# Kernel optimization log

Measured on AMD Instinct MI355X. Metric: run time of the kernel, lower is better.

The kernel has to match this reference:

```python
import jax, jax.numpy as jnp
import numpy as np
import math

B, S, D, H, MLP, L = 4, 1024, 512, 8, 2048, 4
C = D // H  # head dim = 64
K_RATIO = 0.25
TOPK = max(1, min(S, int(math.ceil(K_RATIO * S))))  # 256
EPS = 1e-6


def layernorm(x, w, b):
    mu = jnp.mean(x, axis=-1, keepdims=True)
    var = jnp.mean(jnp.square(x - mu), axis=-1, keepdims=True)
    return (x - mu) * jax.lax.rsqrt(var + EPS) * w + b


def dwconv3(x, w):
    # x: (B, Ch, S), w: (Ch, 1, 3) depthwise conv, padding 1
    return jax.lax.conv_general_dilated(
        x, w, window_strides=(1,), padding=[(1, 1)],
        dimension_numbers=('NCH', 'OIH', 'NCH'),
        feature_group_count=x.shape[1])


def setup_inputs() -> dict:
    key = jax.random.key(0)
    ks = jax.random.split(key, 16)
    g = lambda k, shape, s=0.02: jax.random.normal(k, shape, jnp.float32) * s
    return {
        'x': jax.random.normal(ks[0], (B, S, D), jnp.float32),
        'pos_emb': g(ks[1], (1, S, D)),
        'ln1_w': jnp.ones((L, D), jnp.float32),
        'ln1_b': jnp.zeros((L, D), jnp.float32),
        'qkv_w': g(ks[2], (L, 3 * D, D)),
        'dw_w': g(ks[3], (L, 3 * D, 1, 3), 0.1),
        'temp': jnp.ones((L, H), jnp.float32),
        'proj_w': g(ks[4], (L, D, D)),
        'ln2_w': jnp.ones((L, D), jnp.float32),
        'ln2_b': jnp.zeros((L, D), jnp.float32),
        'mlp_w1': g(ks[5], (L, MLP, D)),
        'mlp_b1': g(ks[6], (L, MLP), 1e-6),
        'mlp_w2': g(ks[7], (L, D, MLP)),
        'mlp_b2': g(ks[8], (L, D), 1e-6),
        'lnf_w': jnp.ones((D,), jnp.float32),
        'lnf_b': jnp.zeros((D,), jnp.float32),
    }


def _block(x, ln1_w, ln1_b, qkv_w, dw_w, temp, proj_w, ln2_w, ln2_b,
           mlp_w1, mlp_b1, mlp_w2, mlp_b2):
    # x: (B, S, D)
    h = layernorm(x, ln1_w, ln1_b).swapaxes(1, 2)        # (B, D, S)
    qkv = jnp.einsum('od,bds->bos', qkv_w, h)            # (B, 3D, S) 1x1 conv
    qkv = dwconv3(qkv, dw_w)                             # depthwise k=3
    q, k, v = jnp.split(qkv, 3, axis=1)                  # each (B, D, S)
    # 'b (head c) s -> b head s c'
    to_heads = lambda t: t.reshape(B, H, C, S).transpose(0, 1, 3, 2)
    q, k, v = to_heads(q), to_heads(k), to_heads(v)      # (B, H, S, C)
    q = q / jnp.maximum(jnp.linalg.norm(q, axis=-1, keepdims=True), 1e-12)
    k = k / jnp.maximum(jnp.linalg.norm(k, axis=-1, keepdims=True), 1e-12)
    scores = jnp.einsum('bhsc,bhtc->bhst', q, k) * temp[None, :, None, None]
    # top-k per query row: keep entries >= k-th largest, mask rest to -inf
    kth = jax.lax.top_k(scores, TOPK)[0][..., -1:]       # (B, H, S, 1)
    sparse = jnp.where(scores >= kth, scores, -jnp.inf)
    sparse = jnp.clip(sparse, -10000.0, 10000.0)         # -inf -> -10000
    attn = jax.nn.softmax(sparse, axis=-1)
    out = jnp.einsum('bhst,bhtc->bhsc', attn, v)         # (B, H, S, C)
    out = out.transpose(0, 1, 3, 2).reshape(B, D, S)     # 'b head s c -> b (head c) s'
    out = jnp.einsum('od,bds->bos', proj_w, out)         # project_out 1x1 conv
    x = x + out.swapaxes(1, 2)                           # residual (dropout=0)
    y = layernorm(x, ln2_w, ln2_b)
    y = jax.nn.gelu(y @ mlp_w1.T + mlp_b1, approximate=False) @ mlp_w2.T + mlp_b2
    return x + y


def reference(x, pos_emb, ln1_w, ln1_b, qkv_w, dw_w, temp, proj_w,
              ln2_w, ln2_b, mlp_w1, mlp_b1, mlp_w2, mlp_b2, lnf_w, lnf_b):
    h = x + pos_emb
    for i in range(L):
        h = _block(h, ln1_w[i], ln1_b[i], qkv_w[i], dw_w[i], temp[i], proj_w[i],
                   ln2_w[i], ln2_b[i], mlp_w1[i], mlp_b1[i], mlp_w2[i], mlp_b2[i])
    return layernorm(h, lnf_w, lnf_b)
```

## Files before the change

kernel.cpp:

```cpp
#include <hip/hip_runtime.h>

#define NB   4
#define SEQ  1024
#define DIM  512
#define NH   8
#define HD   64
#define MLPD 2048
#define NL   4
#define TOPKK 256
#define QKVD 1536
#define QT   16

typedef short bh8 __attribute__((ext_vector_type(8)));
typedef float f32x4 __attribute__((ext_vector_type(4)));

__device__ __forceinline__ float b2f(unsigned short v) {
    return __uint_as_float(((unsigned)v) << 16);
}
__device__ __forceinline__ unsigned short f2b(float f) {
    unsigned u = __float_as_uint(f);
    u += 0x7FFFu + ((u >> 16) & 1u);
    return (unsigned short)(u >> 16);
}
__device__ __forceinline__ float ldin(const void* p, size_t i, int bf) {
    return bf ? b2f(((const unsigned short*)p)[i]) : ((const float*)p)[i];
}
__device__ __forceinline__ float wave_sum(float v) {
#pragma unroll
    for (int m = 32; m; m >>= 1) v += __shfl_xor(v, m);
    return v;
}
__device__ __forceinline__ unsigned f2key16(unsigned short u) {
    return (u & 0x8000u) ? (unsigned)((~u) & 0xFFFFu) : (unsigned)(u | 0x8000u);
}
__device__ __forceinline__ unsigned short key16b(unsigned k) {
    return (k & 0x8000u) ? (unsigned short)(k & 0x7FFFu)
                         : (unsigned short)((~k) & 0xFFFFu);
}
__device__ __forceinline__ uint4 pack8(const float* __restrict__ p) {
    uint4 r;
    r.x = (unsigned)f2b(p[0]) | ((unsigned)f2b(p[1]) << 16);
    r.y = (unsigned)f2b(p[2]) | ((unsigned)f2b(p[3]) << 16);
    r.z = (unsigned)f2b(p[4]) | ((unsigned)f2b(p[5]) << 16);
    r.w = (unsigned)f2b(p[6]) | ((unsigned)f2b(p[7]) << 16);
    return r;
}
__device__ __forceinline__ void async16(unsigned short* lds, const unsigned short* g) {
    __builtin_amdgcn_global_load_lds(
        (const __attribute__((address_space(1))) unsigned int*)g,
        (__attribute__((address_space(3))) unsigned int*)lds, 16, 0, 0);
}


__global__ void detect_kernel(const unsigned short* __restrict__ ln1w,
                              int* __restrict__ flag) {
    if (threadIdx.x == 0 && blockIdx.x == 0)
        *flag = (ln1w[0] == 0x3F80u) ? 1 : 0;
}

__global__ __launch_bounds__(256) void wcvt_kernel(
    const void* __restrict__ W, unsigned short* __restrict__ out,
    int n, const int* __restrict__ dflag) {
    int bf = *dflag;
    int idx = blockIdx.x * 256 + threadIdx.x;
    if (idx < n) out[idx] = f2b(ldin(W, idx, bf));
}

__global__ __launch_bounds__(256) void addpos_kernel(
    const void* __restrict__ x, const void* __restrict__ pos,
    float* __restrict__ h, const int* __restrict__ dflag) {
    int bf = *dflag;
    int idx = blockIdx.x * 256 + threadIdx.x;
    int sd = idx & (SEQ * DIM - 1);
    h[idx] = ldin(x, idx, bf) + ldin(pos, sd, bf);
}

__global__ __launch_bounds__(256) void ln_kernel(
    const float* __restrict__ in, const void* __restrict__ w,
    const void* __restrict__ bb, size_t wo, unsigned short* __restrict__ out,
    const int* __restrict__ dflag) {
    int bf = *dflag;
    __shared__ float red[4];
    int row = blockIdx.x, tid = threadIdx.x;
    int lane = tid & 63, wid = tid >> 6;
    const float* p = in + (size_t)row * DIM;
    float x0 = p[tid], x1 = p[tid + 256];
    float s = wave_sum(x0 + x1);
    if (!lane) red[wid] = s;
    __syncthreads();
    float mean = (red[0] + red[1] + red[2] + red[3]) * (1.0f / DIM);
    float d0 = x0 - mean, d1 = x1 - mean;
    float q = wave_sum(d0 * d0 + d1 * d1);
    __syncthreads();
    if (!lane) red[wid] = q;
    __syncthreads();
    float var = (red[0] + red[1] + red[2] + red[3]) * (1.0f / DIM);
    float rs = rsqrtf(var + 1e-6f);
    unsigned short* o = out + (size_t)row * DIM;
    o[tid]       = f2b(d0 * rs * ldin(w, wo + tid, bf) + ldin(bb, wo + tid, bf));
    o[tid + 256] = f2b(d1 * rs * ldin(w, wo + tid + 256, bf) + ldin(bb, wo + tid + 256, bf));
}

__global__ __launch_bounds__(256) void lnf_kernel(
    const float* __restrict__ in, const void* __restrict__ w,
    const void* __restrict__ bb, void* __restrict__ out,
    const int* __restrict__ dflag) {
    int bf = *dflag;
    __shared__ float red[4];
    int row = blockIdx.x, tid = threadIdx.x;
    int lane = tid & 63, wid = tid >> 6;
    const float* p = in + (size_t)row * DIM;
    float x0 = p[tid], x1 = p[tid + 256];
    float s = wave_sum(x0 + x1);
    if (!lane) red[wid] = s;
    __syncthreads();
    float mean = (red[0] + red[1] + red[2] + red[3]) * (1.0f / DIM);
    float d0 = x0 - mean, d1 = x1 - mean;
    float q = wave_sum(d0 * d0 + d1 * d1);
    __syncthreads();
    if (!lane) red[wid] = q;
    __syncthreads();
    float var = (red[0] + red[1] + red[2] + red[3]) * (1.0f / DIM);
    float rs = rsqrtf(var + 1e-6f);
    float v0 = d0 * rs * ldin(w, tid, bf) + ldin(bb, tid, bf);
    float v1 = d1 * rs * ldin(w, tid + 256, bf) + ldin(bb, tid + 256, bf);
    size_t o = (size_t)row * DIM;
    if (bf) {
        ((unsigned short*)out)[o + tid]       = f2b(v0);
        ((unsigned short*)out)[o + tid + 256] = f2b(v1);
    } else {
        ((float*)out)[o + tid]       = v0;
        ((float*)out)[o + tid + 256] = v1;
    }
}

__global__ __launch_bounds__(256) void gemm_mfma_kernel(
    const unsigned short* __restrict__ A, const void* __restrict__ W, size_t wo,
    const void* __restrict__ bias, size_t bo, void* __restrict__ C,
    int M, int N, int K, int flags, const int* __restrict__ dflag) {
    int bf = *dflag;
    __shared__ unsigned short As[128 * 32];
    __shared__ unsigned short Bs[128 * 32];
    int tid = threadIdx.x;
    int w = tid >> 6, l = tid & 63;
    int n0 = blockIdx.x * 128, m0 = blockIdx.y * 128;
    int wm = (w >> 1) * 64, wn = (w & 1) * 64;
    int lq = l & 15, lk = l >> 4;

    int srow = w * 32 + (l >> 2);
    int cb = (l & 3) * 8;
    const unsigned short* aG = A + (size_t)(m0 + srow) * K + cb;
    size_t wb = wo + (size_t)(n0 + srow) * K + cb;
    unsigned short* sA0 = &As[w * 1024 + l * 8];
    unsigned short* sA1 = &As[w * 1024 + 512 + l * 8];
    unsigned short* sB0 = &Bs[w * 1024 + l * 8];
    unsigned short* sB1 = &Bs[w * 1024 + 512 + l * 8];

    f32x4 acc[4][4];
#pragma unroll
    for (int i = 0; i < 4; ++i)
#pragma unroll
        for (int j = 0; j < 4; ++j)
            acc[i][j] = (f32x4){0.f, 0.f, 0.f, 0.f};

    for (int k0 = 0; k0 < K; k0 += 32) {
        uint4 a0 = *(const uint4*)(aG + k0);
        uint4 a1 = *(const uint4*)(aG + 16 * K + k0);
        uint4 b0, b1;
        if (bf) {
            b0 = *(const uint4*)((const unsigned short*)W + wb + k0);
            b1 = *(const uint4*)((const unsigned short*)W + wb + 16 * K + k0);
        } else {
            b0 = pack8((const float*)W + wb + k0);
            b1 = pack8((const float*)W + wb + 16 * K + k0);
        }
        __syncthreads();
        *(uint4*)sA0 = a0;
        *(uint4*)sA1 = a1;
        *(uint4*)sB0 = b0;
        *(uint4*)sB1 = b1;
        __syncthreads();
        bh8 af[4], bw[4];
#pragma unroll
        for (int i = 0; i < 4; ++i) {
            af[i] = *(const bh8*)&As[(wm + i * 16 + lq) * 32 + lk * 8];
            bw[i] = *(const bh8*)&Bs[(wn + i * 16 + lq) * 32 + lk * 8];
        }
#pragma unroll
        for (int i = 0; i < 4; ++i)
#pragma unroll
            for (int j = 0; j < 4; ++j)
                acc[i][j] = __builtin_amdgcn_mfma_f32_16x16x32_bf16(
                    af[i], bw[j], acc[i][j], 0, 0, 0);
    }

    int lr4 = lk * 4;
#pragma unroll
    for (int i = 0; i < 4; ++i) {
#pragma unroll
        for (int j = 0; j < 4; ++j) {
            int n = n0 + wn + j * 16 + lq;
            float bv = (flags & 4) ? ldin(bias, bo + n, bf) : 0.0f;
#pragma unroll
            for (int r = 0; r < 4; ++r) {
                int m = m0 + wm + i * 16 + lr4 + r;
                float v = acc[i][j][r] + bv;
                if (flags & 2) v = 0.5f * v * (1.0f + erff(v * 0.70710678118654752f));
                size_t o = (size_t)m * N + n;
                if (flags & 1) ((float*)C)[o] += v;
                else           ((unsigned short*)C)[o] = f2b(v);
            }
        }
    }
}

__global__ __launch_bounds__(256) void gemm_mfma_n64_kernel(
    const unsigned short* __restrict__ A, const void* __restrict__ W, size_t wo,
    const void* __restrict__ bias, size_t bo, void* __restrict__ C,
    int M, int N, int K, int flags, const int* __restrict__ dflag) {
    int bf = *dflag;
    __shared__ unsigned short As[128 * 32];
    __shared__ unsigned short Bs[64 * 32];
    int tid = threadIdx.x;
    int w = tid >> 6, l = tid & 63;
    int n0 = blockIdx.x * 64, m0 = blockIdx.y * 128;
    int wm = (w >> 1) * 64, wn = (w & 1) * 32;
    int lq = l & 15, lk = l >> 4;

    int srowA = w * 32 + (l >> 2);
    int cb = (l & 3) * 8;
    const unsigned short* aG = A + (size_t)(m0 + srowA) * K + cb;
    int srowB = w * 16 + (l >> 2);
    size_t wb = wo + (size_t)(n0 + srowB) * K + cb;
    unsigned short* sA0 = &As[w * 1024 + l * 8];
    unsigned short* sA1 = &As[w * 1024 + 512 + l * 8];
    unsigned short* sB0 = &Bs[w * 512 + l * 8];

    f32x4 acc[4][2];
#pragma unroll
    for (int i = 0; i < 4; ++i) {
        acc[i][0] = (f32x4){0.f, 0.f, 0.f, 0.f};
        acc[i][1] = (f32x4){0.f, 0.f, 0.f, 0.f};
    }

    for (int k0 = 0; k0 < K; k0 += 32) {
        uint4 a0 = *(const uint4*)(aG + k0);
        uint4 a1 = *(const uint4*)(aG + 16 * K + k0);
        uint4 b0;
        if (bf) b0 = *(const uint4*)((const unsigned short*)W + wb + k0);
        else    b0 = pack8((const float*)W + wb + k0);
        __syncthreads();
        *(uint4*)sA0 = a0;
        *(uint4*)sA1 = a1;
        *(uint4*)sB0 = b0;
        __syncthreads();
        bh8 af[4], bw[2];
#pragma unroll
        for (int i = 0; i < 4; ++i)
            af[i] = *(const bh8*)&As[(wm + i * 16 + lq) * 32 + lk * 8];
        bw[0] = *(const bh8*)&Bs[(wn + lq) * 32 + lk * 8];
        bw[1] = *(const bh8*)&Bs[(wn + 16 + lq) * 32 + lk * 8];
#pragma unroll
        for (int i = 0; i < 4; ++i) {
            acc[i][0] = __builtin_amdgcn_mfma_f32_16x16x32_bf16(af[i], bw[0], acc[i][0], 0, 0, 0);
            acc[i][1] = __builtin_amdgcn_mfma_f32_16x16x32_bf16(af[i], bw[1], acc[i][1], 0, 0, 0);
        }
    }

    int lr4 = lk * 4;
#pragma unroll
    for (int i = 0; i < 4; ++i) {
#pragma unroll
        for (int j = 0; j < 2; ++j) {
            int n = n0 + wn + j * 16 + lq;
            float bv = (flags & 4) ? ldin(bias, bo + n, bf) : 0.0f;
#pragma unroll
            for (int r = 0; r < 4; ++r) {
                int m = m0 + wm + i * 16 + lr4 + r;
                float v = acc[i][j][r] + bv;
                if (flags & 2) v = 0.5f * v * (1.0f + erff(v * 0.70710678118654752f));
                size_t o = (size_t)m * N + n;
                if (flags & 1) ((float*)C)[o] += v;
                else           ((unsigned short*)C)[o] = f2b(v);
            }
        }
    }
}

__global__ __launch_bounds__(256) void gemm_n64_dlds_kernel(
    const unsigned short* __restrict__ A, const unsigned short* __restrict__ W, size_t wo,
    const void* __restrict__ bias, size_t bo, void* __restrict__ C,
    int M, int N, int K, int flags, const int* __restrict__ dflag) {
    __shared__ unsigned short As[128 * 32];
    __shared__ unsigned short Bs[64 * 32];
    int tid = threadIdx.x;
    int w = tid >> 6, l = tid & 63;
    int n0 = blockIdx.x * 64, m0 = blockIdx.y * 128;
    int kz = blockIdx.z;
    int Ks = K / (int)gridDim.z;
    int kbeg = kz * Ks, kend = kbeg + Ks;
    int wm = (w >> 1) * 64, wn = (w & 1) * 32;
    int lq = l & 15, lk = l >> 4;

    int srowA = w * 32 + (l >> 2);
    int srowB = w * 16 + (l >> 2);
    int cb = (l & 3) * 8;
    const unsigned short* aG = A + (size_t)(m0 + srowA) * K + cb;
    const unsigned short* wG = W + wo + (size_t)(n0 + srowB) * K + cb;
    unsigned short* lA0 = As + w * 1024;
    unsigned short* lA1 = As + w * 1024 + 512;
    unsigned short* lB0 = Bs + w * 512;

    f32x4 acc[4][2];
#pragma unroll
    for (int i = 0; i < 4; ++i) {
        acc[i][0] = (f32x4){0.f, 0.f, 0.f, 0.f};
        acc[i][1] = (f32x4){0.f, 0.f, 0.f, 0.f};
    }

    for (int k0 = kbeg; k0 < kend; k0 += 32) {
        __syncthreads();
        async16(lA0, aG + k0);
        async16(lA1, aG + 16 * K + k0);
        async16(lB0, wG + k0);
        __syncthreads();
        bh8 af[4], bw[2];
#pragma unroll
        for (int i = 0; i < 4; ++i)
            af[i] = *(const bh8*)&As[(wm + i * 16 + lq) * 32 + lk * 8];
        bw[0] = *(const bh8*)&Bs[(wn + lq) * 32 + lk * 8];
        bw[1] = *(const bh8*)&Bs[(wn + 16 + lq) * 32 + lk * 8];
#pragma unroll
        for (int i = 0; i < 4; ++i) {
            acc[i][0] = __builtin_amdgcn_mfma_f32_16x16x32_bf16(af[i], bw[0], acc[i][0], 0, 0, 0);
            acc[i][1] = __builtin_amdgcn_mfma_f32_16x16x32_bf16(af[i], bw[1], acc[i][1], 0, 0, 0);
        }
    }

    int bf = (flags & 4) ? *dflag : 0;
    int lr4 = lk * 4;
#pragma unroll
    for (int i = 0; i < 4; ++i) {
#pragma unroll
        for (int j = 0; j < 2; ++j) {
            int n = n0 + wn + j * 16 + lq;
            float bv = ((flags & 4) && kz == 0) ? ldin(bias, bo + n, bf) : 0.0f;
#pragma unroll
            for (int r = 0; r < 4; ++r) {
                int m = m0 + wm + i * 16 + lr4 + r;
                float v = acc[i][j][r] + bv;
                if (flags & 2) v = 0.5f * v * (1.0f + erff(v * 0.70710678118654752f));
                size_t o = (size_t)m * N + n;
                if (flags & 8)      atomicAdd(&((float*)C)[o], v);
                else if (flags & 1) ((float*)C)[o] += v;
                else                ((unsigned short*)C)[o] = f2b(v);
            }
        }
    }
}

__global__ __launch_bounds__(256) void dwqkv_kernel(
    const unsigned short* __restrict__ in, const void* __restrict__ w, size_t wo,
    const void* __restrict__ temp, size_t to,
    unsigned short* __restrict__ qn, unsigned short* __restrict__ Kc,
    unsigned short* __restrict__ Vt, const int* __restrict__ dflag) {
    int bf = *dflag;
    int tid = threadIdx.x;
    int g = tid >> 6, c = tid & 63;
    int gid = blockIdx.x * 4 + g;
    int h = gid & 7;
    int bs = gid >> 3;
    int s = bs & (SEQ - 1), b = bs >> 10;
    int bh = b * NH + h;
    const unsigned short* row = in + (size_t)bs * QKVD;
    float vals[3];
#pragma unroll
    for (int t = 0; t < 3; ++t) {
        int o = t * 512 + h * HD + c;
        float w0 = ldin(w, wo + o * 3 + 0, bf);
        float w1 = ldin(w, wo + o * 3 + 1, bf);
        float w2 = ldin(w, wo + o * 3 + 2, bf);
        float a = w1 * b2f(row[o]);
        if (s > 0)       a += w0 * b2f(row[o - QKVD]);
        if (s < SEQ - 1) a += w2 * b2f(row[o + QKVD]);
        vals[t] = a;
    }
    float qs = wave_sum(vals[0] * vals[0]);
    float ks = wave_sum(vals[1] * vals[1]);
    float t_ = ldin(temp, to + h, bf);
    qn[(size_t)bs * DIM + h * HD + c] = f2b(vals[0] / fmaxf(sqrtf(qs), 1e-12f) * t_);
    Kc[((size_t)bh * SEQ + s) * HD + c] = f2b(vals[1] / fmaxf(sqrtf(ks), 1e-12f));
    Vt[(((size_t)bh * 32 + (s >> 5)) * HD + c) * 32 + (s & 31)] = f2b(vals[2]);
}

__global__ __launch_bounds__(256) void attn_kernel(
    const unsigned short* __restrict__ q, const unsigned short* __restrict__ Kc,
    const unsigned short* __restrict__ Vt, unsigned short* __restrict__ outp) {
    __shared__ __align__(16) unsigned short sc16[QT * 1024];

    int tid = threadIdx.x;
    int w = tid >> 6, l = tid & 63;
    int lq = l & 15, lk = l >> 4;
    int bid = blockIdx.x;
    int qt = bid & 63;
    int h = (bid >> 6) & 7;
    int b = bid >> 9;
    int bh = b * NH + h;

    const unsigned short* qp = q + (size_t)(b * SEQ + qt * QT + lq) * DIM + h * HD + lk * 8;
    bh8 aq0 = *(const bh8*)(qp);
    bh8 aq1 = *(const bh8*)(qp + 32);

    const unsigned short* Kbh = Kc + (size_t)bh * SEQ * HD;
    int wi = lq & 7;
    for (int kb = 0; kb < 16; ++kb) {
        int key0 = (w * 16 + kb) * 16;
        const unsigned short* kp = Kbh + (size_t)(key0 + lq) * HD + lk * 8;
        bh8 b0 = *(const bh8*)(kp);
        bh8 b1 = *(const bh8*)(kp + 32);
        f32x4 acc = {0.f, 0.f, 0.f, 0.f};
        acc = __builtin_amdgcn_mfma_f32_16x16x32_bf16(aq0, b0, acc, 0, 0, 0);
        acc = __builtin_amdgcn_mfma_f32_16x16x32_bf16(aq1, b1, acc, 0, 0, 0);
        int chunk = (key0 + lq) >> 3;
#pragma unroll
        for (int r = 0; r < 4; ++r) {
            int row = lk * 4 + r;
            int sw = (row ^ (row >> 2)) & 7;
            sc16[row * 1024 + ((chunk ^ sw) << 3) + wi] = f2b(acc[r]);
        }
    }
    __syncthreads();

    for (int rr = 0; rr < 4; ++rr) {
        int row = w * 4 + rr;
        unsigned short* srow = sc16 + row * 1024;
        uint4 r0 = *(const uint4*)&srow[l * 8];
        uint4 r1 = *(const uint4*)&srow[512 + l * 8];
        unsigned wd[8] = {r0.x, r0.y, r0.z, r0.w, r1.x, r1.y, r1.z, r1.w};
        float v[16];
#pragma unroll
        for (int j = 0; j < 8; ++j) {
            v[2 * j]     = __uint_as_float(wd[j] << 16);
            v[2 * j + 1] = __uint_as_float(wd[j] & 0xFFFF0000u);
        }
        float m = v[0];
#pragma unroll
        for (int j = 1; j < 16; ++j) m = fmaxf(m, v[j]);
#pragma unroll
        for (int off = 1; off < 64; off <<= 1) m = fmaxf(m, __shfl_xor(m, off));
        m = fminf(fmaxf(m, -10000.f), 10000.f);
        unsigned T = 0;
        for (int bit = 15; bit >= 0; --bit) {
            unsigned cand = T | (1u << bit);
            float tf = b2f(key16b(cand));
            unsigned cnt = 0;
#pragma unroll
            for (int j = 0; j < 16; ++j)
                cnt += (unsigned)__popcll(__ballot(v[j] >= tf));
            if (cnt >= TOPKK) T = cand;
        }
        float kth = b2f(key16b(T));
        float ssum = 0.f;
#pragma unroll
        for (int j = 0; j < 16; ++j) {
            float a = fminf(fmaxf(v[j], -10000.f), 10000.f);
            float ev = (v[j] >= kth) ? __expf(a - m) : 0.0f;
            ssum += ev;
            v[j] = ev;
        }
#pragma unroll
        for (int off = 1; off < 64; off <<= 1) ssum += __shfl_xor(ssum, off);
        float inv = 1.0f / ssum;
        unsigned pw[8];
#pragma unroll
        for (int j = 0; j < 8; ++j) {
            float e0 = v[2 * j] * inv, e1 = v[2 * j + 1] * inv;
            unsigned r;
            asm("v_cvt_pk_bf16_f32 %0, %1, %2" : "=v"(r) : "v"(e0), "v"(e1));
            pw[j] = r;
        }
        *(uint4*)&srow[l * 8]       = (uint4){pw[0], pw[1], pw[2], pw[3]};
        *(uint4*)&srow[512 + l * 8] = (uint4){pw[4], pw[5], pw[6], pw[7]};
    }
    __syncthreads();

    {
        const unsigned short* Vbh = Vt + (size_t)bh * SEQ * HD;
        const unsigned short* prow = sc16 + lq * 1024;
        int swq = (lq ^ (lq >> 2)) & 7;
        f32x4 oacc = {0.f, 0.f, 0.f, 0.f};
        for (int tc = 0; tc < 32; ++tc) {
            bh8 ap = *(const bh8*)&prow[((tc * 4 + lk) ^ swq) << 3];
            bh8 bv = *(const bh8*)(Vbh + (size_t)tc * 2048 + (w * 16 + lq) * 32 + lk * 8);
            oacc = __builtin_amdgcn_mfma_f32_16x16x32_bf16(ap, bv, oacc, 0, 0, 0);
        }
#pragma unroll
        for (int r = 0; r < 4; ++r) {
            int qrow = lk * 4 + r;
            outp[((size_t)(b * SEQ + qt * QT + qrow)) * DIM + h * HD + w * 16 + lq] = f2b(oacc[r]);
        }
    }
}

extern "C" void kernel_launch(void* const* d_in, const int* in_sizes, int n_in,
                              void* d_out, int out_size, void* d_ws, size_t ws_size,
                              hipStream_t stream) {
    (void)in_sizes; (void)n_in; (void)out_size;
    const void* x     = d_in[0];
    const void* pos   = d_in[1];
    const void* ln1w  = d_in[2];
    const void* ln1b  = d_in[3];
    const void* qkvw  = d_in[4];
    const void* dww   = d_in[5];
    const void* temp  = d_in[6];
    const void* projw = d_in[7];
    const void* ln2w  = d_in[8];
    const void* ln2b  = d_in[9];
    const void* w1    = d_in[10];
    const void* b1    = d_in[11];
    const void* w2    = d_in[12];
    const void* b2    = d_in[13];
    const void* lnfw  = d_in[14];
    const void* lnfb  = d_in[15];

    float* wsf = (float*)d_ws;
    const size_t M1 = (size_t)1024 * 1024;
    float*          h    = wsf;
    unsigned short* bn   = (unsigned short*)(wsf + 2 * M1);
    unsigned short* C2   = (unsigned short*)(wsf + 3 * M1);
    unsigned short* Vt   = (unsigned short*)(wsf + 6 * M1);
    unsigned short* Kc   = (unsigned short*)(wsf + 7 * M1);
    unsigned short* Mb   = C2;
    int*            flag = (int*)(wsf + 9 * M1);
    unsigned short* Wc   = (unsigned short*)(wsf + 9 * M1 + 16);

    const int MTOK  = NB * SEQ;
    const int nQKVW = NL * QKVD * DIM;
    const int nPROJ = NL * DIM * DIM;
    const int nW1   = NL * MLPD * DIM;
    const int nW2   = NL * DIM * MLPD;
    const size_t wcElems = (size_t)nQKVW + nPROJ + nW1 + nW2;
    const int big = ws_size >= ((9 * M1 + 16) * 4 + wcElems * 2);

    unsigned short* WcQ  = Wc;
    unsigned short* WcP  = Wc + nQKVW;
    unsigned short* WcW1 = Wc + nQKVW + nPROJ;
    unsigned short* WcW2 = Wc + nQKVW + nPROJ + (size_t)nW1;

    detect_kernel<<<1, 64, 0, stream>>>((const unsigned short*)ln1w, flag);
    addpos_kernel<<<(NB * SEQ * DIM) / 256, 256, 0, stream>>>(x, pos, h, flag);

    if (big) {
        wcvt_kernel<<<nQKVW / 256, 256, 0, stream>>>(qkvw, WcQ, nQKVW, flag);
        wcvt_kernel<<<nPROJ / 256, 256, 0, stream>>>(projw, WcP, nPROJ, flag);
        wcvt_kernel<<<nW1 / 256, 256, 0, stream>>>(w1, WcW1, nW1, flag);
        wcvt_kernel<<<nW2 / 256, 256, 0, stream>>>(w2, WcW2, nW2, flag);
    }

    for (int l = 0; l < NL; ++l) {
        ln_kernel<<<MTOK, 256, 0, stream>>>(h, ln1w, ln1b, (size_t)l * DIM, bn, flag);
        if (big) {
            gemm_n64_dlds_kernel<<<dim3(QKVD / 64, MTOK / 128, 1), 256, 0, stream>>>(
                bn, WcQ, (size_t)l * QKVD * DIM, nullptr, 0, C2,
                MTOK, QKVD, DIM, 0, flag);
        } else {
            gemm_mfma_kernel<<<dim3(QKVD / 128, MTOK / 128), 256, 0, stream>>>(
                bn, qkvw, (size_t)l * QKVD * DIM, nullptr, 0, C2,
                MTOK, QKVD, DIM, 0, flag);
        }
        dwqkv_kernel<<<(NB * SEQ * NH) / 4, 256, 0, stream>>>(
            C2, dww, (size_t)l * QKVD * 3, temp, (size_t)l * NH, bn, Kc, Vt, flag);
        attn_kernel<<<NB * NH * (SEQ / QT), 256, 0, stream>>>(bn, Kc, Vt, bn);
        if (big) {
            gemm_n64_dlds_kernel<<<dim3(DIM / 64, MTOK / 128, 2), 256, 0, stream>>>(
                bn, WcP, (size_t)l * DIM * DIM, nullptr, 0, h,
                MTOK, DIM, DIM, 8, flag);
        } else {
            gemm_mfma_n64_kernel<<<dim3(DIM / 64, MTOK / 128), 256, 0, stream>>>(
                bn, projw, (size_t)l * DIM * DIM, nullptr, 0, h,
                MTOK, DIM, DIM, 1, flag);
        }
        ln_kernel<<<MTOK, 256, 0, stream>>>(h, ln2w, ln2b, (size_t)l * DIM, bn, flag);
        if (big) {
            gemm_n64_dlds_kernel<<<dim3(MLPD / 64, MTOK / 128, 1), 256, 0, stream>>>(
                bn, WcW1, (size_t)l * MLPD * DIM, b1, (size_t)l * MLPD, Mb,
                MTOK, MLPD, DIM, 2 | 4, flag);
            gemm_n64_dlds_kernel<<<dim3(DIM / 64, MTOK / 128, 2), 256, 0, stream>>>(
                Mb, WcW2, (size_t)l * DIM * MLPD, b2, (size_t)l * DIM, h,
                MTOK, DIM, MLPD, 8 | 4, flag);
        } else {
            gemm_mfma_kernel<<<dim3(MLPD / 128, MTOK / 128), 256, 0, stream>>>(
                bn, w1, (size_t)l * MLPD * DIM, b1, (size_t)l * MLPD, Mb,
                MTOK, MLPD, DIM, 2 | 4, flag);
            gemm_mfma_n64_kernel<<<dim3(DIM / 64, MTOK / 128), 256, 0, stream>>>(
                Mb, w2, (size_t)l * DIM * MLPD, b2, (size_t)l * DIM, h,
                MTOK, DIM, MLPD, 1 | 4, flag);
        }
    }

    lnf_kernel<<<MTOK, 256, 0, stream>>>(h, lnfw, lnfb, d_out, flag);
}
```

Measured before the change: 1.014 ms.

## Add 128x128-tile direct-LDS GEMM for QKV and MLP-up; remap attention block order

Adds a GEMM kernel with 128x128 output tiles where each wave computes a 64x64 sub-tile (4x4 MFMAs per k-step). It is used for the QKV projection and the first MLP layer to raise arithmetic intensity and reuse of the A and B fragments relative to the 64-wide N tiles. The attention kernel's block index is remapped so that consecutive blocks cycle over heads within a batch instead of over query tiles, which changes cache locality for the K and V reads. The larger tiles halve the grid size and raise register pressure, which may lower occupancy.

```diff
diff --git a/kernel.cpp b/kernel.cpp
--- a/kernel.cpp
+++ b/kernel.cpp
@@ -354,6 +354,76 @@
                 if (flags & 8)      atomicAdd(&((float*)C)[o], v);
                 else if (flags & 1) ((float*)C)[o] += v;
                 else                ((unsigned short*)C)[o] = f2b(v);
+            }
+        }
+    }
+}
+
+__global__ __launch_bounds__(256) void gemm_n128_dlds_kernel(
+    const unsigned short* __restrict__ A, const unsigned short* __restrict__ W, size_t wo,
+    const void* __restrict__ bias, size_t bo, void* __restrict__ C,
+    int M, int N, int K, int flags, const int* __restrict__ dflag) {
+    __shared__ unsigned short As[128 * 32];
+    __shared__ unsigned short Bs[128 * 32];
+    int tid = threadIdx.x;
+    int w = tid >> 6, l = tid & 63;
+    int n0 = blockIdx.x * 128, m0 = blockIdx.y * 128;
+    int wm = (w >> 1) * 64, wn = (w & 1) * 64;
+    int lq = l & 15, lk = l >> 4;
+
+    int srow = w * 32 + (l >> 2);
+    int cb = (l & 3) * 8;
+    const unsigned short* aG = A + (size_t)(m0 + srow) * K + cb;
+    const unsigned short* wG = W + wo + (size_t)(n0 + srow) * K + cb;
+    unsigned short* lA0 = As + w * 1024;
+    unsigned short* lA1 = As + w * 1024 + 512;
+    unsigned short* lB0 = Bs + w * 1024;
+    unsigned short* lB1 = Bs + w * 1024 + 512;
+
+    f32x4 acc[4][4];
+#pragma unroll
+    for (int i = 0; i < 4; ++i)
+#pragma unroll
+        for (int j = 0; j < 4; ++j)
+            acc[i][j] = (f32x4){0.f, 0.f, 0.f, 0.f};
+
+    for (int k0 = 0; k0 < K; k0 += 32) {
+        __syncthreads();
+        async16(lA0, aG + k0);
+        async16(lA1, aG + 16 * K + k0);
+        async16(lB0, wG + k0);
+        async16(lB1, wG + 16 * K + k0);
+        __syncthreads();
+        bh8 af[4], bw[4];
+#pragma unroll
+        for (int i = 0; i < 4; ++i) {
+            af[i] = *(const bh8*)&As[(wm + i * 16 + lq) * 32 + lk * 8];
+            bw[i] = *(const bh8*)&Bs[(wn + i * 16 + lq) * 32 + lk * 8];
+        }
+#pragma unroll
+        for (int i = 0; i < 4; ++i)
+#pragma unroll
+            for (int j = 0; j < 4; ++j)
+                acc[i][j] = __builtin_amdgcn_mfma_f32_16x16x32_bf16(
+                    af[i], bw[j], acc[i][j], 0, 0, 0);
+    }
+
+    int bf = (flags & 4) ? *dflag : 0;
+    int lr4 = lk * 4;
+#pragma unroll
+    for (int i = 0; i < 4; ++i) {
+#pragma unroll
+        for (int j = 0; j < 4; ++j) {
+            int n = n0 + wn + j * 16 + lq;
+            float bv = (flags & 4) ? ldin(bias, bo + n, bf) : 0.0f;
+#pragma unroll
+            for (int r = 0; r < 4; ++r) {
+                int m = m0 + wm + i * 16 + lr4 + r;
+                float v = acc[i][j][r] + bv;
+                if (flags & 2) v = 0.5f * v * (1.0f + erff(v * 0.70710678118654752f));
+                size_t o = (size_t)m * N + n;
+                if (flags & 1) ((float*)C)[o] += v;
+                else           ((unsigned short*)C)[o] = f2b(v);
             }
         }
     }
@@ -402,10 +472,10 @@
     int w = tid >> 6, l = tid & 63;
     int lq = l & 15, lk = l >> 4;
     int bid = blockIdx.x;
-    int qt = bid & 63;
-    int h = (bid >> 6) & 7;
-    int b = bid >> 9;
-    int bh = b * NH + h;
+    int qt = (bid >> 3) & 63;
+    int bh = ((bid >> 9) << 3) | (bid & 7);
+    int h = bh & 7;
+    int b = bh >> 3;
 
     const unsigned short* qp = q + (size_t)(b * SEQ + qt * QT + lq) * DIM + h * HD + lk * 8;
     bh8 aq0 = *(const bh8*)(qp);
@@ -560,7 +630,7 @@
     for (int l = 0; l < NL; ++l) {
         ln_kernel<<<MTOK, 256, 0, stream>>>(h, ln1w, ln1b, (size_t)l * DIM, bn, flag);
         if (big) {
-            gemm_n64_dlds_kernel<<<dim3(QKVD / 64, MTOK / 128, 1), 256, 0, stream>>>(
+            gemm_n128_dlds_kernel<<<dim3(QKVD / 128, MTOK / 128), 256, 0, stream>>>(
                 bn, WcQ, (size_t)l * QKVD * DIM, nullptr, 0, C2,
                 MTOK, QKVD, DIM, 0, flag);
         } else {
@@ -582,7 +652,7 @@
         }
         ln_kernel<<<MTOK, 256, 0, stream>>>(h, ln2w, ln2b, (size_t)l * DIM, bn, flag);
         if (big) {
-            gemm_n64_dlds_kernel<<<dim3(MLPD / 64, MTOK / 128, 1), 256, 0, stream>>>(
+            gemm_n128_dlds_kernel<<<dim3(MLPD / 128, MTOK / 128), 256, 0, stream>>>(
                 bn, WcW1, (size_t)l * MLPD * DIM, b1, (size_t)l * MLPD, Mb,
                 MTOK, MLPD, DIM, 2 | 4, flag);
             gemm_n64_dlds_kernel<<<dim3(DIM / 64, MTOK / 128, 2), 256, 0, stream>>>(
```

Result: slower. 1.042 ms (+2.8%).

## Transpose QK MFMA to write packed score rows and remap attention blocks

Applied to the files above, without the earlier changes.

Swaps the MFMA operand order in the score computation so each lane holds four consecutive keys for one query row. This lets scores be packed with v_cvt_pk and written as 8-byte LDS stores instead of scalar 2-byte stores, using a new 4-element swizzle granularity. The same swizzle is applied to the PV reads. The block index mapping is changed so consecutive blocks cycle over heads rather than query tiles, and the QK and PV loops are unrolled by two to expose more loads per iteration. The aim is to cut LDS store count and bank conflicts in the attention kernel, at the cost of more register pressure and a changed L2 access pattern for K/V.

```diff
diff --git a/kernel.cpp b/kernel.cpp
--- a/kernel.cpp
+++ b/kernel.cpp
@@ -36,6 +36,11 @@
 __device__ __forceinline__ unsigned short key16b(unsigned k) {
     return (k & 0x8000u) ? (unsigned short)(k & 0x7FFFu)
                          : (unsigned short)((~k) & 0xFFFFu);
+}
+__device__ __forceinline__ unsigned cvtpk(float a, float b) {
+    unsigned r;
+    asm("v_cvt_pk_bf16_f32 %0, %1, %2" : "=v"(r) : "v"(a), "v"(b));
+    return r;
 }
 __device__ __forceinline__ uint4 pack8(const float* __restrict__ p) {
     uint4 r;
@@ -402,32 +407,38 @@
     int w = tid >> 6, l = tid & 63;
     int lq = l & 15, lk = l >> 4;
     int bid = blockIdx.x;
-    int qt = bid & 63;
-    int h = (bid >> 6) & 7;
-    int b = bid >> 9;
-    int bh = b * NH + h;
+    int qt = (bid >> 3) & 63;
+    int bh = ((bid >> 9) << 3) | (bid & 7);
+    int h = bh & 7;
+    int b = bh >> 3;
 
     const unsigned short* qp = q + (size_t)(b * SEQ + qt * QT + lq) * DIM + h * HD + lk * 8;
     bh8 aq0 = *(const bh8*)(qp);
     bh8 aq1 = *(const bh8*)(qp + 32);
 
+    int swz = ((lq ^ (lq >> 2)) & 7) << 1;
+
     const unsigned short* Kbh = Kc + (size_t)bh * SEQ * HD;
-    int wi = lq & 7;
-    for (int kb = 0; kb < 16; ++kb) {
+    unsigned short* srowq = sc16 + lq * 1024;
+    for (int kb = 0; kb < 16; kb += 2) {
         int key0 = (w * 16 + kb) * 16;
-        const unsigned short* kp = Kbh + (size_t)(key0 + lq) * HD + lk * 8;
-        bh8 b0 = *(const bh8*)(kp);
-        bh8 b1 = *(const bh8*)(kp + 32);
-        f32x4 acc = {0.f, 0.f, 0.f, 0.f};
-        acc = __builtin_amdgcn_mfma_f32_16x16x32_bf16(aq0, b0, acc, 0, 0, 0);
-        acc = __builtin_amdgcn_mfma_f32_16x16x32_bf16(aq1, b1, acc, 0, 0, 0);
-        int chunk = (key0 + lq) >> 3;
-#pragma unroll
-        for (int r = 0; r < 4; ++r) {
-            int row = lk * 4 + r;
-            int sw = (row ^ (row >> 2)) & 7;
-            sc16[row * 1024 + ((chunk ^ sw) << 3) + wi] = f2b(acc[r]);
-        }
+        const unsigned short* kp0 = Kbh + (size_t)(key0 + lq) * HD + lk * 8;
+        const unsigned short* kp1 = kp0 + 16 * HD;
+        bh8 b0 = *(const bh8*)(kp0);
+        bh8 b1 = *(const bh8*)(kp0 + 32);
+        bh8 b2 = *(const bh8*)(kp1);
+        bh8 b3 = *(const bh8*)(kp1 + 32);
+        f32x4 a0 = {0.f, 0.f, 0.f, 0.f};
+        f32x4 a1 = {0.f, 0.f, 0.f, 0.f};
+        a0 = __builtin_amdgcn_mfma_f32_16x16x32_bf16(b0, aq0, a0, 0, 0, 0);
+        a0 = __builtin_amdgcn_mfma_f32_16x16x32_bf16(b1, aq1, a0, 0, 0, 0);
+        a1 = __builtin_amdgcn_mfma_f32_16x16x32_bf16(b2, aq0, a1, 0, 0, 0);
+        a1 = __builtin_amdgcn_mfma_f32_16x16x32_bf16(b3, aq1, a1, 0, 0, 0);
+        int c0 = (key0 >> 2) + lk;
+        uint2 w0 = {cvtpk(a0[0], a0[1]), cvtpk(a0[2], a0[3])};
+        uint2 w1 = {cvtpk(a1[0], a1[1]), cvtpk(a1[2], a1[3])};
+        *(uint2*)&srowq[(c0 ^ swz) << 2]       = w0;
+        *(uint2*)&srowq[((c0 + 4) ^ swz) << 2] = w1;
     }
     __syncthreads();
 
@@ -473,12 +484,8 @@
         float inv = 1.0f / ssum;
         unsigned pw[8];
 #pragma unroll
-        for (int j = 0; j < 8; ++j) {
-            float e0 = v[2 * j] * inv, e1 = v[2 * j + 1] * inv;
-            unsigned r;
-            asm("v_cvt_pk_bf16_f32 %0, %1, %2" : "=v"(r) : "v"(e0), "v"(e1));
-            pw[j] = r;
-        }
+        for (int j = 0; j < 8; ++j)
+            pw[j] = cvtpk(v[2 * j] * inv, v[2 * j + 1] * inv);
         *(uint4*)&srow[l * 8]       = (uint4){pw[0], pw[1], pw[2], pw[3]};
         *(uint4*)&srow[512 + l * 8] = (uint4){pw[4], pw[5], pw[6], pw[7]};
     }
@@ -487,12 +494,15 @@
     {
         const unsigned short* Vbh = Vt + (size_t)bh * SEQ * HD;
         const unsigned short* prow = sc16 + lq * 1024;
-        int swq = (lq ^ (lq >> 2)) & 7;
         f32x4 oacc = {0.f, 0.f, 0.f, 0.f};
-        for (int tc = 0; tc < 32; ++tc) {
-            bh8 ap = *(const bh8*)&prow[((tc * 4 + lk) ^ swq) << 3];
-            bh8 bv = *(const bh8*)(Vbh + (size_t)tc * 2048 + (w * 16 + lq) * 32 + lk * 8);
-            oacc = __builtin_amdgcn_mfma_f32_16x16x32_bf16(ap, bv, oacc, 0, 0, 0);
+        for (int tc = 0; tc < 32; tc += 2) {
+            const unsigned short* vp0 = Vbh + (size_t)tc * 2048 + (w * 16 + lq) * 32 + lk * 8;
+            bh8 bv0 = *(const bh8*)(vp0);
+            bh8 bv1 = *(const bh8*)(vp0 + 2048);
+            bh8 ap0 = *(const bh8*)&prow[((tc * 8 + lk * 2) ^ swz) << 2];
+            bh8 ap1 = *(const bh8*)&prow[(((tc + 1) * 8 + lk * 2) ^ swz) << 2];
+            oacc = __builtin_amdgcn_mfma_f32_16x16x32_bf16(ap0, bv0, oacc, 0, 0, 0);
+            oacc = __builtin_amdgcn_mfma_f32_16x16x32_bf16(ap1, bv1, oacc, 0, 0, 0);
         }
 #pragma unroll
         for (int r = 0; r < 4; ++r) {
```

Result: no change. 999.1 us (-1.4%).
